# Kernel tuning notes

Measured on AMD Instinct MI355X. Metric: run time of the kernel, lower is better.

Reference implementation:

```python
import jax, jax.numpy as jnp
import numpy as np
import math

def _eq_conv1x1(x, w):
    # EqualizedConv2d: 1x1 conv, no bias, weight scaled by sqrt(2 / fan_in) at runtime.
    scale = math.sqrt(2.0 / w.shape[1])
    return jnp.einsum('bchw,oc->bohw', x, w * scale)

def _maxpool2x2(x):
    b, c, h, w = x.shape
    return x.reshape(b, c, h // 2, 2, w // 2, 2).max(axis=(3, 5))

def setup_inputs() -> dict:
    key = jax.random.key(0)
    ks = jax.random.split(key, 6)
    B, Cin, H, W = 8, 256, 64, 64
    Cout = 512
    return {
        'x': jax.random.normal(ks[0], (B, Cin, H, W), dtype=jnp.float32),
        'w_theta': jax.random.normal(ks[1], (Cout // 8, Cin), dtype=jnp.float32),
        'w_phi': jax.random.normal(ks[2], (Cout // 8, Cin), dtype=jnp.float32),
        'w_g': jax.random.normal(ks[3], (Cout // 2, Cin), dtype=jnp.float32),
        'w_o': jax.random.normal(ks[4], (Cout, Cout // 2), dtype=jnp.float32),
        'w_res': jax.random.normal(ks[5], (Cout, Cin), dtype=jnp.float32),
        'gamma': jnp.ones((1,), dtype=jnp.float32),
    }

def reference(x, w_theta, w_phi, w_g, w_o, w_res, gamma):
    B, _, H, W = x.shape
    theta = _eq_conv1x1(x, w_theta).reshape(B, -1, H * W)          # [B, Co/8, HW]
    phi = _maxpool2x2(_eq_conv1x1(x, w_phi)).reshape(B, -1, H * W // 4)  # [B, Co/8, HW/4]
    g = _maxpool2x2(_eq_conv1x1(x, w_g)).reshape(B, -1, H * W // 4)      # [B, Co/2, HW/4]
    # attention: softmax over key dim (no 1/sqrt(d) scaling, as in the original)
    scores = jnp.einsum('bcn,bcm->bnm', theta, phi)                # [B, HW, HW/4]
    beta = jax.nn.softmax(scores, axis=-1)
    att = jnp.einsum('bcm,bnm->bcn', g, beta).reshape(B, -1, H, W)  # [B, Co/2, H, W]
    out = _eq_conv1x1(att, w_o)                                     # [B, Co, H, W]
    res = _eq_conv1x1(x, w_res)
    inv_sqrt2 = jnp.float32(1.0 / math.sqrt(2.0))
    return (gamma[0] * out + res) * inv_sqrt2
```

## Files before the change

### kernel.cpp

```cpp
#include <hip/hip_runtime.h>


typedef _Float16 f16;
typedef f16 f16x2 __attribute__((ext_vector_type(2)));
typedef f16 f16x4 __attribute__((ext_vector_type(4)));
typedef f16 f16x8 __attribute__((ext_vector_type(8)));
typedef float f32x4 __attribute__((ext_vector_type(4)));

#define MFMA16(a, b, c) __builtin_amdgcn_mfma_f32_16x16x32_f16((a), (b), (c), 0, 0, 0)

__device__ __forceinline__ void gload16(const void* src, void* dst_lds) {
  __builtin_amdgcn_global_load_lds(
      (const __attribute__((address_space(1))) void*)src,
      (__attribute__((address_space(3))) void*)dst_lds, 16, 0, 0);
}

__global__ __launch_bounds__(256, 4)
void k_prep_w(const float* __restrict__ wt, const float* __restrict__ wp,
              const float* __restrict__ wg, const float* __restrict__ wo,
              const float* __restrict__ wr, const float* __restrict__ gamma,
              f16* __restrict__ Wproj, f16* __restrict__ Wcat) {
  int i = blockIdx.x * 256 + threadIdx.x;
  const float s = 0.08838834764831845f;
  const float is2 = 0.7071067811865476f;
  if (i < 384 * 256) {
    float v = (i < 64 * 256) ? wt[i]
              : (i < 128 * 256 ? wp[i - 64 * 256] : wg[i - 128 * 256]);
    Wproj[i] = (f16)(v * s);
  } else {
    int j = i - 384 * 256;
    if (j < 512 * 512) {
      int r = j >> 9, c = j & 511;
      float v = (c < 256) ? wo[r * 256 + c] * (gamma[0] * s * is2)
                          : wr[r * 256 + (c - 256)] * (s * is2);
      Wcat[j] = (f16)v;
    }
  }
}

__global__ __launch_bounds__(256, 4)
void k_transpose(const float* __restrict__ x, f16* __restrict__ xT) {
  __shared__ f16 tile[64 * 72];
  int b = blockIdx.z, nt = blockIdx.y, ct = blockIdx.x;
  int t = threadIdx.x;
  {
    int c = t >> 2, nch = (t & 3) * 16;
    const float* src = x + (((size_t)b * 256 + ct * 64 + c) << 12) + nt * 64 + nch;
    float4 v0 = *(const float4*)(src);
    float4 v1 = *(const float4*)(src + 4);
    float4 v2 = *(const float4*)(src + 8);
    float4 v3 = *(const float4*)(src + 12);
    f16x8 a = {(f16)v0.x, (f16)v0.y, (f16)v0.z, (f16)v0.w,
               (f16)v1.x, (f16)v1.y, (f16)v1.z, (f16)v1.w};
    f16x8 bb = {(f16)v2.x, (f16)v2.y, (f16)v2.z, (f16)v2.w,
                (f16)v3.x, (f16)v3.y, (f16)v3.z, (f16)v3.w};
    *(f16x8*)&tile[c * 72 + nch] = a;
    *(f16x8*)&tile[c * 72 + nch + 8] = bb;
  }
  __syncthreads();
  {
    int n = t >> 2, cch = (t & 3) * 16;
    f16 tmp[16];
#pragma unroll
    for (int i = 0; i < 16; i++) tmp[i] = tile[(cch + i) * 72 + n];
    f16x8 a, bb;
#pragma unroll
    for (int i = 0; i < 8; i++) { a[i] = tmp[i]; bb[i] = tmp[8 + i]; }
    f16* dst = xT + (((size_t)b * 4096 + nt * 64 + n) << 8) + ct * 64 + cch;
    *(f16x8*)dst = a;
    *(f16x8*)(dst + 8) = bb;
  }
}

__global__ __launch_bounds__(256, 2)
void k_gemm_projq(const f16* __restrict__ xT, const f16* __restrict__ Wproj,
                  f16* __restrict__ Q, f16* __restrict__ Kp, f16* __restrict__ V) {
  __shared__ f16 lds[192 * 64];
  f16* Alds = lds;
  f16* Blds = lds + 64 * 64;
  int b = blockIdx.z, mt = blockIdx.y, nt = blockIdx.x;
  int tid = threadIdx.x;
  int lane = tid & 63, wave = tid >> 6;
  int wm = wave >> 1, wn = wave & 1;
  int l15 = lane & 15, hi = lane >> 4;
  f32x4 acc[2][4];
#pragma unroll
  for (int mf = 0; mf < 2; mf++)
#pragma unroll
    for (int nf = 0; nf < 4; nf++) acc[mf][nf] = (f32x4){0, 0, 0, 0};
  const f16* Abase = Wproj + ((mt * 64) << 8);
  const f16* Bbase = xT + (((size_t)b * 4096 + nt * 128) << 8);
  for (int k0 = 0; k0 < 256; k0 += 64) {
    __syncthreads();
#pragma unroll
    for (int i = 0; i < 2; i++) {
      int chunk = i * 256 + tid;
      int row = chunk >> 3, cc = chunk & 7, scc = cc ^ (row & 7);
      gload16(Abase + (row << 8) + k0 + scc * 8, (char*)Alds + (i * 256 + wave * 64) * 16);
    }
#pragma unroll
    for (int i = 0; i < 4; i++) {
      int chunk = i * 256 + tid;
      int row = chunk >> 3, cc = chunk & 7, scc = cc ^ (row & 7);
      gload16(Bbase + (row << 8) + k0 + scc * 8, (char*)Blds + (i * 256 + wave * 64) * 16);
    }
    __syncthreads();
#pragma unroll
    for (int ks = 0; ks < 2; ks++) {
      int cb = (hi * 8 + ks * 32) * 2;
      f16x8 af[2], bf[4];
#pragma unroll
      for (int mf = 0; mf < 2; mf++) {
        int row = wm * 32 + mf * 16 + l15;
        af[mf] = *(const f16x8*)((const char*)Alds + row * 128 + (cb ^ ((row & 7) << 4)));
      }
#pragma unroll
      for (int nf = 0; nf < 4; nf++) {
        int row = wn * 64 + nf * 16 + l15;
        bf[nf] = *(const f16x8*)((const char*)Blds + row * 128 + (cb ^ ((row & 7) << 4)));
      }
#pragma unroll
      for (int mf = 0; mf < 2; mf++)
#pragma unroll
        for (int nf = 0; nf < 4; nf++) acc[mf][nf] = MFMA16(af[mf], bf[nf], acc[mf][nf]);
    }
  }
  if (mt == 0) {
#pragma unroll
    for (int mf = 0; mf < 2; mf++)
#pragma unroll
      for (int nf = 0; nf < 4; nf++)
#pragma unroll
        for (int r = 0; r < 4; r++) {
          int jl = wm * 32 + mf * 16 + hi * 4 + r;
          int n = nt * 128 + wn * 64 + nf * 16 + l15;
          Q[(((size_t)b * 4096 + n) << 6) + jl] = (f16)acc[mf][nf][r];
        }
  } else {
    __syncthreads();
    f16* Pool = lds;
#pragma unroll
    for (int mf = 0; mf < 2; mf++)
#pragma unroll
      for (int nf = 0; nf < 4; nf++)
#pragma unroll
        for (int r = 0; r < 4; r++) {
          int jl = wm * 32 + mf * 16 + hi * 4 + r;
          int col = wn * 64 + nf * 16 + l15;
          Pool[jl * 132 + col] = (f16)acc[mf][nf][r];
        }
    __syncthreads();
    if (mt == 1) {
      int m_l = tid >> 3;
      int jj8 = (tid & 7) * 8;
      f16x8 w;
#pragma unroll
      for (int i = 0; i < 8; i++) {
        int jj = jj8 + i;
        f16x2 p0 = *(const f16x2*)&Pool[jj * 132 + 2 * m_l];
        f16x2 p1 = *(const f16x2*)&Pool[jj * 132 + 64 + 2 * m_l];
        float v = fmaxf(fmaxf((float)p0[0], (float)p0[1]),
                        fmaxf((float)p1[0], (float)p1[1]));
        w[i] = (f16)v;
      }
      *(f16x8*)&Kp[((size_t)b * 1024 + nt * 32 + m_l) * 64 + jj8] = w;
    } else {
      int ch_l = tid >> 2;
      int m8 = (tid & 3) * 8;
      f16x8 w;
#pragma unroll
      for (int i = 0; i < 8; i++) {
        int mm = m8 + i;
        f16x2 p0 = *(const f16x2*)&Pool[ch_l * 132 + 2 * mm];
        f16x2 p1 = *(const f16x2*)&Pool[ch_l * 132 + 64 + 2 * mm];
        float v = fmaxf(fmaxf((float)p0[0], (float)p0[1]),
                        fmaxf((float)p1[0], (float)p1[1]));
        w[i] = (f16)v;
      }
      int ch = (mt - 2) * 64 + ch_l;
      *(f16x8*)&V[(((size_t)b * 256 + ch) << 10) + nt * 32 + m8] = w;
    }
  }
}

__global__ __launch_bounds__(512, 4)
void k_flash(const f16* __restrict__ Q, const f16* __restrict__ Kp,
             const f16* __restrict__ V, f16* __restrict__ att) {
  __shared__ f16 Klds[64 * 64];
  __shared__ f16 Vlds[256 * 64];
  __shared__ f16 Plds[4][16 * 72];
  int b = blockIdx.y, qt = blockIdx.x;
  int tid = threadIdx.x;
  int lane = tid & 63, wave = tid >> 6;
  int rg = wave >> 1, cg2 = wave & 1;
  int l15 = lane & 15, hi = lane >> 4;
  const f16* Kb = Kp + ((size_t)b << 16);
  const f16* Vb = V + ((size_t)b << 18);
  f16* Pw = &Plds[rg][0];
  const float L2E = 1.44269504f;
  f16x8 qf[2];
#pragma unroll
  for (int ks = 0; ks < 2; ks++)
    qf[ks] = *(const f16x8*)(
        Q + (((size_t)b * 4096 + qt * 64 + rg * 16 + l15) << 6) + ks * 32 + hi * 8);
  f32x4 o[8];
#pragma unroll
  for (int i = 0; i < 8; i++) o[i] = (f32x4){0, 0, 0, 0};
  float mrow = -1e30f, lrow = 0.f;

  int cbase = hi * 16;

#define STAGE(kt)                                                                \
  {                                                                              \
    {                                                                            \
      int chunk = tid;                                                           \
      int row = chunk >> 3, cc = chunk & 7, scc = cc ^ (row & 7);                \
      gload16(Kb + (((kt) * 64 + row) << 6) + scc * 8,                           \
              (char*)&Klds[0] + chunk * 16);                                     \
    }                                                                            \
    _Pragma("unroll") for (int i = 0; i < 4; i++) {                              \
      int chunk = i * 512 + tid;                                                 \
      int row = chunk >> 3, cc = chunk & 7, scc = cc ^ (row & 7);                \
      gload16(Vb + ((size_t)row << 10) + (kt) * 64 + scc * 8,                    \
              (char*)&Vlds[0] + chunk * 16);                                     \
    }                                                                            \
  }

  STAGE(0);
  __syncthreads();
  for (int kt = 0; kt < 16; ++kt) {
    f32x4 s[4];
#pragma unroll
    for (int mf = 0; mf < 4; mf++) s[mf] = (f32x4){0, 0, 0, 0};
#pragma unroll
    for (int ks = 0; ks < 2; ks++) {
      f16x8 kf[4];
#pragma unroll
      for (int mf = 0; mf < 4; mf++) {
        int row = mf * 16 + l15;
        kf[mf] = *(const f16x8*)((const char*)&Klds[0] + row * 128 +
                                 ((cbase + ks * 64) ^ ((row & 7) << 4)));
      }
#pragma unroll
      for (int mf = 0; mf < 4; mf++) s[mf] = MFMA16(kf[mf], qf[ks], s[mf]);
    }
    float t0 = fmaxf(fmaxf(s[0][0], s[1][0]), fmaxf(s[2][0], s[3][0]));
    float t1 = fmaxf(fmaxf(s[0][1], s[1][1]), fmaxf(s[2][1], s[3][1]));
    float t2 = fmaxf(fmaxf(s[0][2], s[1][2]), fmaxf(s[2][2], s[3][2]));
    float t3 = fmaxf(fmaxf(s[0][3], s[1][3]), fmaxf(s[2][3], s[3][3]));
    float mx = fmaxf(fmaxf(t0, t1), fmaxf(t2, t3));
    mx = fmaxf(mx, __shfl_xor(mx, 16, 64));
    mx = fmaxf(mx, __shfl_xor(mx, 32, 64));
    if (__any(mx > mrow + 8.f)) {
      float mnew = fmaxf(mrow, mx);
      float corr = __builtin_amdgcn_exp2f((mrow - mnew) * L2E);
      lrow *= corr;
      mrow = mnew;
#pragma unroll
      for (int r = 0; r < 4; r++) {
        float cr = __shfl(corr, (hi << 4) + (hi << 2) + r, 64);
#pragma unroll
        for (int cf = 0; cf < 8; cf++) o[cf][r] *= cr;
      }
    }
    {
      float e[4][4];
#pragma unroll
      for (int mf = 0; mf < 4; mf++)
#pragma unroll
        for (int r = 0; r < 4; r++)
          e[mf][r] = __builtin_amdgcn_exp2f((s[mf][r] - mrow) * L2E);
#pragma unroll
      for (int mf = 0; mf < 4; mf++) {
        f16x4 w = {(f16)e[mf][0], (f16)e[mf][1], (f16)e[mf][2], (f16)e[mf][3]};
        *(f16x4*)((char*)Pw + l15 * 144 + mf * 32 + hi * 8) = w;
      }
      float u0 = (e[0][0] + e[1][0]) + (e[2][0] + e[3][0]);
      float u1 = (e[0][1] + e[1][1]) + (e[2][1] + e[3][1]);
      float u2 = (e[0][2] + e[1][2]) + (e[2][2] + e[3][2]);
      float u3 = (e[0][3] + e[1][3]) + (e[2][3] + e[3][3]);
      float sum = (u0 + u1) + (u2 + u3);
      sum += __shfl_xor(sum, 16, 64);
      sum += __shfl_xor(sum, 32, 64);
      lrow += sum;
    }
#pragma unroll
    for (int ks = 0; ks < 2; ks++) {
      f16x8 af = *(const f16x8*)((char*)Pw + l15 * 144 + ks * 64 + hi * 16);
      __builtin_amdgcn_s_setprio(1);
#pragma unroll
      for (int cg = 0; cg < 2; cg++) {
        f16x8 vf[4];
#pragma unroll
        for (int u = 0; u < 4; u++) {
          int row = (cg2 * 8 + cg * 4 + u) * 16 + l15;
          vf[u] = *(const f16x8*)((const char*)&Vlds[0] + row * 128 +
                                  ((cbase + ks * 64) ^ ((row & 7) << 4)));
        }
#pragma unroll
        for (int u = 0; u < 4; u++) o[cg * 4 + u] = MFMA16(af, vf[u], o[cg * 4 + u]);
      }
      __builtin_amdgcn_s_setprio(0);
    }
    if (kt < 15) {
      __syncthreads();
      STAGE(kt + 1);
      __syncthreads();
    }
  }
#undef STAGE
  int nbase = qt * 64 + rg * 16 + hi * 4;
  float inv = 1.f / lrow;
#pragma unroll
  for (int r = 0; r < 4; r++) {
    float iv = __shfl(inv, (hi << 4) + (hi << 2) + r, 64);
#pragma unroll
    for (int cf = 0; cf < 8; cf++) {
      int n = nbase + r;
      int c = cg2 * 128 + cf * 16 + l15;
      att[(((size_t)b * 4096 + n) << 8) + c] = (f16)(o[cf][r] * iv);
    }
  }
}

__global__ __launch_bounds__(256, 2)
void k_gemm_out(const f16* __restrict__ Wcat, const f16* __restrict__ att,
                const f16* __restrict__ xT, float* __restrict__ out) {
  __shared__ f16 Alds[128 * 64];
  __shared__ f16 Blds[128 * 64];
  int b = blockIdx.z, mt = blockIdx.y, nt = blockIdx.x;
  int lane = threadIdx.x & 63, wave = threadIdx.x >> 6;
  int wm = wave >> 1, wn = wave & 1;
  f32x4 acc[4][4];
#pragma unroll
  for (int mf = 0; mf < 4; mf++)
#pragma unroll
    for (int nf = 0; nf < 4; nf++) acc[mf][nf] = (f32x4){0, 0, 0, 0};
  const f16* Abase = Wcat + (size_t)(mt * 128) * 512;
  for (int k0 = 0; k0 < 512; k0 += 64) {
    __syncthreads();
#pragma unroll
    for (int i = 0; i < 4; i++) {
      int chunk = i * 256 + threadIdx.x;
      int row = chunk >> 3, cc = chunk & 7, scc = cc ^ (row & 7);
      gload16(Abase + row * 512 + k0 + scc * 8, (char*)Alds + (i * 256 + wave * 64) * 16);
    }
    const f16* Bcol = (k0 < 256) ? (att + (((size_t)b * 4096 + nt * 128) << 8))
                                 : (xT + (((size_t)b * 4096 + nt * 128) << 8));
    int kk = (k0 < 256) ? k0 : (k0 - 256);
#pragma unroll
    for (int i = 0; i < 4; i++) {
      int chunk = i * 256 + threadIdx.x;
      int row = chunk >> 3, cc = chunk & 7, scc = cc ^ (row & 7);
      gload16(Bcol + (row << 8) + kk + scc * 8, (char*)Blds + (i * 256 + wave * 64) * 16);
    }
    __syncthreads();
#pragma unroll
    for (int ks = 0; ks < 2; ks++) {
      int cb = ((lane >> 4) * 8 + ks * 32) * 2;
      f16x8 af[4], bf[4];
#pragma unroll
      for (int mf = 0; mf < 4; mf++) {
        int row = wm * 64 + mf * 16 + (lane & 15);
        af[mf] = *(const f16x8*)((const char*)Alds + row * 128 + (cb ^ ((row & 7) << 4)));
      }
#pragma unroll
      for (int nf = 0; nf < 4; nf++) {
        int row = wn * 64 + nf * 16 + (lane & 15);
        bf[nf] = *(const f16x8*)((const char*)Blds + row * 128 + (cb ^ ((row & 7) << 4)));
      }
#pragma unroll
      for (int mf = 0; mf < 4; mf++)
#pragma unroll
        for (int nf = 0; nf < 4; nf++) acc[mf][nf] = MFMA16(af[mf], bf[nf], acc[mf][nf]);
    }
  }
#pragma unroll
  for (int mf = 0; mf < 4; mf++)
#pragma unroll
    for (int nf = 0; nf < 4; nf++)
#pragma unroll
      for (int r = 0; r < 4; r++) {
        int oo = mt * 128 + wm * 64 + mf * 16 + (lane >> 4) * 4 + r;
        int n = nt * 128 + wn * 64 + nf * 16 + (lane & 15);
        out[(((size_t)b * 512 + oo) << 12) + n] = acc[mf][nf][r];
      }
}

extern "C" void kernel_launch(void* const* d_in, const int* in_sizes, int n_in,
                              void* d_out, int out_size, void* d_ws, size_t ws_size,
                              hipStream_t stream) {
  const float* x = (const float*)d_in[0];
  const float* wt = (const float*)d_in[1];
  const float* wp = (const float*)d_in[2];
  const float* wg = (const float*)d_in[3];
  const float* wo = (const float*)d_in[4];
  const float* wr = (const float*)d_in[5];
  const float* gm = (const float*)d_in[6];
  float* out = (float*)d_out;
  char* ws = (char*)d_ws;
  const size_t MB = 1024 * 1024;
  f16* xT = (f16*)(ws);
  f16* Qb = (f16*)(ws + 16 * MB);
  f16* Kp = (f16*)(ws + 20 * MB);
  f16* Vb = (f16*)(ws + 21 * MB);
  f16* Wproj = (f16*)(ws + 25 * MB);
  f16* Wcat = (f16*)(ws + 25 * MB + 512 * 1024);
  f16* att = (f16*)(ws + 26 * MB);

  hipLaunchKernelGGL(k_prep_w, dim3(1408), dim3(256), 0, stream, wt, wp, wg, wo, wr, gm,
                     Wproj, Wcat);
  hipLaunchKernelGGL(k_transpose, dim3(4, 64, 8), dim3(256), 0, stream, x, xT);
  hipLaunchKernelGGL(k_gemm_projq, dim3(32, 6, 8), dim3(256), 0, stream, xT, Wproj, Qb,
                     Kp, Vb);
  hipLaunchKernelGGL(k_flash, dim3(64, 8), dim3(512), 0, stream, Qb, Kp, Vb, att);
  hipLaunchKernelGGL(k_gemm_out, dim3(32, 4, 8), dim3(256), 0, stream, Wcat, att, xT, out);
}
```

Measured before the change: 108.6 us.

## Prefetch next K/V tile into registers during compute in flash kernel

Replaces the direct global-to-LDS async loads, which were issued after the compute and waited on immediately, with register prefetch. The next tile's K and V are loaded into registers at the start of each iteration, overlapping global latency with the QK/softmax/PV compute. The registers are written to LDS between barriers. This costs about 20 extra VGPRs per thread, which may hurt occupancy at 512 threads with 4 blocks per CU, and adds explicit LDS store instructions.

```diff
diff --git a/kernel.cpp b/kernel.cpp
--- a/kernel.cpp
+++ b/kernel.cpp
@@ -198,6 +198,19 @@
   const f16* Vb = V + ((size_t)b << 18);
   f16* Pw = &Plds[rg][0];
   const float L2E = 1.44269504f;
+  int krow_s = tid >> 3, kcc = tid & 7;
+  int kscc = kcc ^ (krow_s & 7);
+  const f16* kp_src = Kb + (krow_s << 6) + kscc * 8;
+  f16* kp_dst = &Klds[tid * 8];
+  const f16* vp_src[4];
+  f16* vp_dst[4];
+#pragma unroll
+  for (int i = 0; i < 4; i++) {
+    int chunk = i * 512 + tid;
+    int row = chunk >> 3, cc = chunk & 7, scc = cc ^ (row & 7);
+    vp_src[i] = Vb + ((size_t)row << 10) + scc * 8;
+    vp_dst[i] = &Vlds[chunk * 8];
+  }
   f16x8 qf[2];
 #pragma unroll
   for (int ks = 0; ks < 2; ks++)
@@ -210,25 +223,27 @@
 
   int cbase = hi * 16;
 
-#define STAGE(kt)                                                                \
-  {                                                                              \
-    {                                                                            \
-      int chunk = tid;                                                           \
-      int row = chunk >> 3, cc = chunk & 7, scc = cc ^ (row & 7);                \
-      gload16(Kb + (((kt) * 64 + row) << 6) + scc * 8,                           \
-              (char*)&Klds[0] + chunk * 16);                                     \
-    }                                                                            \
-    _Pragma("unroll") for (int i = 0; i < 4; i++) {                              \
-      int chunk = i * 512 + tid;                                                 \
-      int row = chunk >> 3, cc = chunk & 7, scc = cc ^ (row & 7);                \
-      gload16(Vb + ((size_t)row << 10) + (kt) * 64 + scc * 8,                    \
-              (char*)&Vlds[0] + chunk * 16);                                     \
-    }                                                                            \
-  }
-
-  STAGE(0);
+  f16x8 kreg, vreg0, vreg1, vreg2, vreg3;
+  kreg = *(const f16x8*)(kp_src);
+  vreg0 = *(const f16x8*)(vp_src[0]);
+  vreg1 = *(const f16x8*)(vp_src[1]);
+  vreg2 = *(const f16x8*)(vp_src[2]);
+  vreg3 = *(const f16x8*)(vp_src[3]);
+  *(f16x8*)kp_dst = kreg;
+  *(f16x8*)vp_dst[0] = vreg0;
+  *(f16x8*)vp_dst[1] = vreg1;
+  *(f16x8*)vp_dst[2] = vreg2;
+  *(f16x8*)vp_dst[3] = vreg3;
   __syncthreads();
+
   for (int kt = 0; kt < 16; ++kt) {
+    if (kt < 15) {
+      kreg = *(const f16x8*)(kp_src + ((kt + 1) << 12));
+      vreg0 = *(const f16x8*)(vp_src[0] + ((kt + 1) << 6));
+      vreg1 = *(const f16x8*)(vp_src[1] + ((kt + 1) << 6));
+      vreg2 = *(const f16x8*)(vp_src[2] + ((kt + 1) << 6));
+      vreg3 = *(const f16x8*)(vp_src[3] + ((kt + 1) << 6));
+    }
     f32x4 s[4];
 #pragma unroll
     for (int mf = 0; mf < 4; mf++) s[mf] = (f32x4){0, 0, 0, 0};
@@ -304,11 +319,14 @@
     }
     if (kt < 15) {
       __syncthreads();
-      STAGE(kt + 1);
+      *(f16x8*)kp_dst = kreg;
+      *(f16x8*)vp_dst[0] = vreg0;
+      *(f16x8*)vp_dst[1] = vreg1;
+      *(f16x8*)vp_dst[2] = vreg2;
+      *(f16x8*)vp_dst[3] = vreg3;
       __syncthreads();
     }
   }
-#undef STAGE
   int nbase = qt * 64 + rg * 16 + hi * 4;
   float inv = 1.f / lrow;
 #pragma unroll
```

Result: no change. 107.6 us (-0.9%).
